# Performance work log

Measured on AMD Instinct MI355X. Metric: run time of the kernel, lower is better.

The kernel has to match this reference:

```python
import jax, jax.numpy as jnp
import numpy as np

D = 1024
H = 16
HD = D // H  # 64

def setup_inputs() -> dict:
    key = jax.random.key(0)
    ks = jax.random.split(key, 7)
    B, S = 2, 2048
    x = jax.random.normal(ks[0], (B, S, D), dtype=jnp.float32)
    M = jax.random.randint(ks[1], (B, S, S), 0, 2, dtype=jnp.int32)
    s = 1.0 / np.sqrt(D)
    W_q = jax.random.normal(ks[2], (D, D), dtype=jnp.float32) * s
    W_k = jax.random.normal(ks[3], (D, D), dtype=jnp.float32) * s
    W_v = jax.random.normal(ks[4], (D, D), dtype=jnp.float32) * s
    W_o = jax.random.normal(ks[5], (D, D), dtype=jnp.float32) * s
    b_o = jax.random.normal(ks[6], (D,), dtype=jnp.float32) * 0.01
    return {"x": x, "M": M, "W_q": W_q, "W_k": W_k, "W_v": W_v, "W_o": W_o, "b_o": b_o}

def reference(x, M, W_q, W_k, W_v, W_o, b_o):
    B, S, _ = x.shape
    scale = HD ** -0.5
    # project and split heads: [B, H, S, HD]
    def heads(W):
        return (x @ W.T).reshape(B, S, H, HD).transpose(0, 2, 1, 3)
    Q, K, V = heads(W_q), heads(W_k), heads(W_v)
    scores = jnp.einsum('bhqd,bhkd->bhqk', Q, K) * scale
    mask = (M[:, None, :, :] == 0)  # broadcast over heads
    scores = jnp.where(mask, jnp.float32(-1e9), scores)
    A = jax.nn.softmax(scores, axis=-1)
    out = jnp.einsum('bhqk,bhkd->bhqd', A, V)
    out = out.transpose(0, 2, 1, 3).reshape(B, S, D)
    return out @ W_o.T + b_o
```

## Files before the change

### kernel.cpp

```cpp
#include <hip/hip_runtime.h>
#include <hip/hip_bf16.h>

typedef unsigned short u16;
typedef unsigned int u32;
typedef unsigned long long u64;
typedef _Float16 f16;
typedef __attribute__((__ext_vector_type__(4))) _Float16 f16x4;
typedef __attribute__((__ext_vector_type__(8))) short bf16x8;
typedef __attribute__((__ext_vector_type__(4))) float f32x4;
typedef __attribute__((__ext_vector_type__(16))) float f32x16;

__device__ __forceinline__ u16 f2bf(float f) {
    u32 u = __float_as_uint(f);
    return (u16)((u + 0x7fffu + ((u >> 16) & 1u)) >> 16);
}

__device__ __forceinline__ u32 pk2(float e, float o) {
    return (__float_as_uint(e) >> 16) | (__float_as_uint(o) & 0xFFFF0000u);
}

__global__ __launch_bounds__(256) void prep_kernel(
    const float4* __restrict__ x,  const float4* __restrict__ wq,
    const float4* __restrict__ wk, const float4* __restrict__ wv,
    const float4* __restrict__ wo,
    u16* __restrict__ xb, u16* __restrict__ wqb, u16* __restrict__ wkb,
    u16* __restrict__ wvb, u16* __restrict__ wob,
    const int* __restrict__ M, u64* __restrict__ Mb2)
{
    if (blockIdx.x < 8192) {
        int gid = blockIdx.x * 256 + threadIdx.x;
        const float4* src; u16* dst; int off;
        if (gid < 1048576) { src = x; dst = xb; off = gid; }
        else {
            int g = gid - 1048576;
            int sel = g >> 18;
            off = g & 262143;
            src = sel == 0 ? wq : sel == 1 ? wk : sel == 2 ? wv : wo;
            dst = sel == 0 ? wqb : sel == 1 ? wkb : sel == 2 ? wvb : wob;
        }
        float4 f = src[off];
        ushort4 o;
        o.x = f2bf(f.x); o.y = f2bf(f.y); o.z = f2bf(f.z); o.w = f2bf(f.w);
        ((ushort4*)dst)[off] = o;
    } else {
        int wg   = (blockIdx.x - 8192) * 4 + (threadIdx.x >> 6);
        int lane = threadIdx.x & 63;
        int w = wg & 31;
        int q = (wg >> 5) & 2047;
        int b = wg >> 16;
        size_t base = ((size_t)(b * 2048 + q)) * 2048 + w * 64 + lane;
        u64 bits = __ballot(M[base] != 0);
        if (lane == 0) Mb2[(size_t)(b * 32 + w) * 2048 + q] = bits;
    }
}

template<int MODE, int BN>
__global__ __launch_bounds__(256) void gemm_k(
    const u16* __restrict__ Ag, const u16* __restrict__ Bg,
    u16* __restrict__ Cq, u16* __restrict__ Kfr, u16* __restrict__ Vfr,
    float* __restrict__ Cf, const float* __restrict__ bias)
{
    constexpr int Kd = 1024;
    constexpr int NB = BN / 32;
    __shared__ u16 As[128 * 32];
    __shared__ u16 Bs[BN * 32];
    const int tid  = threadIdx.x;
    const int wave = tid >> 6, lane = tid & 63;
    const int quad = lane >> 4, l16 = lane & 15;
    const int n0 = blockIdx.x * BN;
    const int m0 = blockIdx.y * 128;

    const int wm = (wave & 1) * 64, wn = (wave >> 1) * (BN / 2);
    f32x4 acc[4][NB];
    #pragma unroll
    for (int i = 0; i < 4; i++)
        #pragma unroll
        for (int j = 0; j < NB; j++)
            acc[i][j] = (f32x4){0.f, 0.f, 0.f, 0.f};

    const int sr = lane >> 2;
    const int sk = (lane & 3) * 8;
    const int ca0 = wave * 2, ca1 = ca0 + 1;
    const u16* gA0 = Ag + (size_t)(m0 + ca0 * 16 + sr) * Kd + sk;
    const u16* gA1 = Ag + (size_t)(m0 + ca1 * 16 + sr) * Kd + sk;
    u16* lA0 = As + ca0 * 512;
    u16* lA1 = As + ca1 * 512;
    const int cb0 = (BN == 128) ? wave * 2 : wave;
    const u16* gB0 = Bg + (size_t)(n0 + cb0 * 16 + sr) * Kd + sk;
    u16* lB0 = Bs + cb0 * 512;
    const u16* gB1 = (BN == 128) ? Bg + (size_t)(n0 + (cb0 + 1) * 16 + sr) * Kd + sk : nullptr;
    u16* lB1 = (BN == 128) ? Bs + (cb0 + 1) * 512 : nullptr;

    #define GLL16(gp, lp) __builtin_amdgcn_global_load_lds( \
        (const __attribute__((address_space(1))) void*)(gp), \
        (__attribute__((address_space(3))) void*)(lp), 16, 0, 0)

    for (int k0 = 0; k0 < Kd; k0 += 32) {
        __syncthreads();
        GLL16(gA0 + k0, lA0);
        GLL16(gA1 + k0, lA1);
        GLL16(gB0 + k0, lB0);
        if (BN == 128) GLL16(gB1 + k0, lB1);
        __syncthreads();

        bf16x8 af[4], bfr[NB];
        #pragma unroll
        for (int mb = 0; mb < 4; mb++)
            af[mb] = *(const bf16x8*)&As[(wm + mb * 16 + l16) * 32 + quad * 8];
        #pragma unroll
        for (int nb = 0; nb < NB; nb++)
            bfr[nb] = *(const bf16x8*)&Bs[(wn + nb * 16 + l16) * 32 + quad * 8];
        #pragma unroll
        for (int mb = 0; mb < 4; mb++)
            #pragma unroll
            for (int nb = 0; nb < NB; nb++)
                acc[mb][nb] = __builtin_amdgcn_mfma_f32_16x16x32_bf16(
                    af[mb], bfr[nb], acc[mb][nb], 0, 0, 0);
    }
    #undef GLL16

    #pragma unroll
    for (int mb = 0; mb < 4; mb++) {
        #pragma unroll
        for (int nb = 0; nb < NB; nb++) {
            const int row  = m0 + wm + mb * 16 + quad * 4;
            const int col  = n0 + wn + nb * 16 + l16;
            if (MODE == 1) {
                #pragma unroll
                for (int r = 0; r < 4; r++)
                    Cf[(size_t)(row + r) * 1024 + col] = acc[mb][nb][r] + bias[col];
            } else {
                const int region = col >> 10;
                const int ccol = col & 1023;
                const int bb = row >> 11, srow = row & 2047;
                const int kt = srow >> 6;
                const int hh = ccol >> 6, dd = ccol & 63;
                if (region == 0) {
                    #pragma unroll
                    for (int r = 0; r < 4; r++)
                        Cq[(size_t)(row + r) * 1024 + ccol] =
                            f2bf(acc[mb][nb][r] * 0.18033688011112042f);
                } else if (region == 1) {
                    const int t = dd >> 4, hik = (dd >> 3) & 1, j = dd & 7;
                    #pragma unroll
                    for (int r = 0; r < 4; r++) {
                        const int km = (srow + r) & 63;
                        const int kn = km >> 5, l31k = km & 31;
                        const int lanek = hik * 32 + l31k;
                        Kfr[((((size_t)(bb * 16 + hh) * 32 + kt) * 8 + kn * 4 + t) * 64
                             + lanek) * 8 + j] = f2bf(acc[mb][nb][r]);
                    }
                } else {
                    const int kinb = srow & 63;
                    const int t = kinb >> 4, hiv = (kinb >> 3) & 1, jb = kinb & 7;
                    const int nd = dd >> 5, l31v = dd & 31;
                    const int lanev = hiv * 32 + l31v;
                    ushort4 pk;
                    pk.x = f2bf(acc[mb][nb][0]); pk.y = f2bf(acc[mb][nb][1]);
                    pk.z = f2bf(acc[mb][nb][2]); pk.w = f2bf(acc[mb][nb][3]);
                    *(ushort4*)&Vfr[((((size_t)(bb * 16 + hh) * 32 + kt) * 8 + nd * 4 + t) * 64
                                     + lanev) * 8 + jb] = pk;
                }
            }
        }
    }
}

__global__ __launch_bounds__(256) void attn_kernel(
    const u16* __restrict__ Qg, const u16* __restrict__ Kfr, const u16* __restrict__ Vfr,
    const u64* __restrict__ Mb2, f16* __restrict__ Opart, float* __restrict__ Lpart)
{
    const int qt = blockIdx.x >> 1;
    const int kh = blockIdx.x & 1;
    const int h  = blockIdx.y;
    const int b  = blockIdx.z;
    const int tid = threadIdx.x, wave = tid >> 6, lane = tid & 63;
    const int l31 = lane & 31, hi = lane >> 5;

    const int    qrow0 = qt * 128 + wave * 32;
    const int    bh    = b * 16 + h;

    bf16x8 qf[4];
    {
        const u16* qp = Qg + ((size_t)b * 2048 + qrow0 + l31) * 1024 + h * 64 + hi * 8;
        #pragma unroll
        for (int t = 0; t < 4; t++) qf[t] = *(const bf16x8*)(qp + t * 16);
    }

    const u16* kfp = Kfr + (size_t)bh * 131072 + lane * 8;
    const u16* vfp = Vfr + (size_t)bh * 131072 + lane * 8;

    f32x16 oacc0, oacc1;
    #pragma unroll
    for (int i = 0; i < 16; i++) { oacc0[i] = 0.f; oacc1[i] = 0.f; }
    float lsum = 0.f;

    const int kt0 = kh * 16;
    #pragma unroll 1
    for (int kt = kt0; kt < kt0 + 16; kt++) {
        const u64 mwv = Mb2[(size_t)(b * 32 + kt) * 2048 + qrow0 + l31];
        const u32 mlo = ((u32)mwv) >> (hi * 4);
        const u32 mhi = ((u32)(mwv >> 32)) >> (hi * 4);
        const size_t fb = (size_t)(kt * 8) * 512;

        #pragma unroll
        for (int ph = 0; ph < 2; ph++) {
            bf16x8 kf[4], vf[4];
            #pragma unroll
            for (int t = 0; t < 4; t++)
                kf[t] = *(const bf16x8*)(kfp + fb + (size_t)(ph * 4 + t) * 512);
            vf[0] = *(const bf16x8*)(vfp + fb + (size_t)(2 * ph) * 512);
            vf[1] = *(const bf16x8*)(vfp + fb + (size_t)(2 * ph + 1) * 512);
            vf[2] = *(const bf16x8*)(vfp + fb + (size_t)(4 + 2 * ph) * 512);
            vf[3] = *(const bf16x8*)(vfp + fb + (size_t)(4 + 2 * ph + 1) * 512);

            f32x16 s;
            #pragma unroll
            for (int i = 0; i < 16; i++) s[i] = 0.f;
            #pragma unroll
            for (int t = 0; t < 4; t++)
                s = __builtin_amdgcn_mfma_f32_32x32x16_bf16(kf[t], qf[t], s, 0, 0, 0);

            const u32 mm = ph ? mhi : mlo;
            #pragma unroll
            for (int reg = 0; reg < 16; reg++) {
                const int kb2 = (reg & 3) + 8 * (reg >> 2);
                float a = __builtin_amdgcn_exp2f(s[reg]);
                a = ((mm >> kb2) & 1u) ? a : 0.0f;
                s[reg] = a; lsum += a;
            }

            bf16x8 pb[2];
            #pragma unroll
            for (int fl = 0; fl < 2; fl++) {
                const int rb = 8 * fl;
                u32 a0 = pk2(s[rb], s[rb + 1]),     a1 = pk2(s[rb + 2], s[rb + 3]);
                u32 a2 = pk2(s[rb + 4], s[rb + 5]), a3 = pk2(s[rb + 6], s[rb + 7]);
                const u32 r0 = __shfl_xor(a0, 32);
                const u32 r1 = __shfl_xor(a1, 32);
                const u32 r2 = __shfl_xor(a2, 32);
                const u32 r3 = __shfl_xor(a3, 32);
                union { u32 u[4]; bf16x8 v; } fu;
                fu.u[0] = hi ? r2 : a0;
                fu.u[1] = hi ? r3 : a1;
                fu.u[2] = hi ? a2 : r0;
                fu.u[3] = hi ? a3 : r1;
                pb[fl] = fu.v;
            }

            oacc0 = __builtin_amdgcn_mfma_f32_32x32x16_bf16(vf[0], pb[0], oacc0, 0, 0, 0);
            oacc0 = __builtin_amdgcn_mfma_f32_32x32x16_bf16(vf[1], pb[1], oacc0, 0, 0, 0);
            oacc1 = __builtin_amdgcn_mfma_f32_32x32x16_bf16(vf[2], pb[0], oacc1, 0, 0, 0);
            oacc1 = __builtin_amdgcn_mfma_f32_32x32x16_bf16(vf[3], pb[1], oacc1, 0, 0, 0);
        }
    }

    lsum += __shfl_xor(lsum, 32);

    const size_t obase = ((size_t)(kh * 32 + bh) * 2048 + qrow0 + l31) * 64;
    #pragma unroll
    for (int tile = 0; tile < 2; tile++) {
        #pragma unroll
        for (int g = 0; g < 4; g++) {
            const int d0 = tile * 32 + g * 8 + hi * 4;
            f16x4 pkv;
            #pragma unroll
            for (int r = 0; r < 4; r++) {
                const int reg = g * 4 + r;
                pkv[r] = (f16)(tile == 0 ? oacc0[reg] : oacc1[reg]);
            }
            *(f16x4*)&Opart[obase + d0] = pkv;
        }
    }
    Lpart[(size_t)kh * 65536 + bh * 2048 + qrow0 + l31] = lsum;
}

__global__ __launch_bounds__(256) void merge_kernel(
    const f16* __restrict__ Opart, const float* __restrict__ Lpart,
    u16* __restrict__ AO)
{
    const int gid = blockIdx.x * 256 + threadIdx.x;
    const int c4 = gid & 15;
    const int q  = (gid >> 4) & 2047;
    const int bh = gid >> 15;
    const int b  = bh >> 4, h = bh & 15;

    const size_t pbase = ((size_t)bh * 2048 + q) * 64 + c4 * 4;
    f16x4 o0 = *(const f16x4*)&Opart[pbase];
    f16x4 o1 = *(const f16x4*)&Opart[(size_t)32 * 2048 * 64 + pbase];
    const float l = Lpart[(size_t)bh * 2048 + q] +
                    Lpart[(size_t)65536 + bh * 2048 + q];
    const float inv = 1.0f / l;

    ushort4 o;
    o.x = f2bf(((float)o0[0] + (float)o1[0]) * inv);
    o.y = f2bf(((float)o0[1] + (float)o1[1]) * inv);
    o.z = f2bf(((float)o0[2] + (float)o1[2]) * inv);
    o.w = f2bf(((float)o0[3] + (float)o1[3]) * inv);
    *(ushort4*)&AO[((size_t)b * 2048 + q) * 1024 + h * 64 + c4 * 4] = o;
}

extern "C" void kernel_launch(void* const* d_in, const int* in_sizes, int n_in,
                              void* d_out, int out_size, void* d_ws, size_t ws_size,
                              hipStream_t stream)
{
    const float* x  = (const float*)d_in[0];
    const int*   Mm = (const int*)d_in[1];
    const float* Wq = (const float*)d_in[2];
    const float* Wk = (const float*)d_in[3];
    const float* Wv = (const float*)d_in[4];
    const float* Wo = (const float*)d_in[5];
    const float* bo = (const float*)d_in[6];
    float* out = (float*)d_out;

    u16* ws  = (u16*)d_ws;
    u16* xb  = ws;
    u16* wqb = xb  + 4194304;
    u16* wkb = wqb + 1048576;
    u16* wvb = wkb + 1048576;
    u16* wob = wvb + 1048576;
    u16* Qb  = wob + 1048576;
    u16* Kfr = Qb  + 4194304;
    u16* Vfr = Kfr + 4194304;
    u16* AOb = Vfr + 4194304;
    u64* Mb2 = (u64*)(AOb + 4194304);
    f16* Opart = (f16*)(Mb2 + 131072);
    float* Lpart = (float*)(Opart + 8388608);

    prep_kernel<<<40960, 256, 0, stream>>>(
        (const float4*)x, (const float4*)Wq, (const float4*)Wk,
        (const float4*)Wv, (const float4*)Wo, xb, wqb, wkb, wvb, wob,
        Mm, Mb2);

    dim3 g1(24, 32, 1);
    gemm_k<0, 128><<<g1, 256, 0, stream>>>(xb, wqb, Qb, Kfr, Vfr, nullptr, nullptr);

    dim3 g2(32, 16, 2);
    attn_kernel<<<g2, 256, 0, stream>>>(Qb, Kfr, Vfr, Mb2, Opart, Lpart);

    merge_kernel<<<4096, 256, 0, stream>>>(Opart, Lpart, AOb);

    dim3 g3(16, 32, 1);
    gemm_k<1, 64><<<g3, 256, 0, stream>>>(AOb, wob, nullptr, nullptr, nullptr,
                                          out, bo);
}
```

Before: 246.2 us.

## Stage K/V fragment epilogue through LDS and shrink attention blocks to one wave

The QKV GEMM epilogue for the K and V regions now writes bf16 fragments into a shared-memory staging buffer in two passes and then copies them out with contiguous 16-byte stores, replacing scattered 2-byte global writes. Separately, the attention kernel goes from 4 waves per block over 128 query rows to a single wave over 32 rows, with four times as many blocks. This aims at better global write coalescing and finer-grained scheduling of attention work, at the cost of extra barriers in the GEMM epilogue and no sharing of K/V loads across waves.

```diff
diff --git a/kernel.cpp b/kernel.cpp
--- a/kernel.cpp
+++ b/kernel.cpp
@@ -62,8 +62,9 @@
 {
     constexpr int Kd = 1024;
     constexpr int NB = BN / 32;
-    __shared__ u16 As[128 * 32];
-    __shared__ u16 Bs[BN * 32];
+    __shared__ u16 SM[8192];
+    u16* As = SM;
+    u16* Bs = SM + 4096;
     const int tid  = threadIdx.x;
     const int wave = tid >> 6, lane = tid & 63;
     const int quad = lane >> 4, l16 = lane & 15;
@@ -119,54 +120,85 @@
     }
     #undef GLL16
 
-    #pragma unroll
-    for (int mb = 0; mb < 4; mb++) {
-        #pragma unroll
-        for (int nb = 0; nb < NB; nb++) {
-            const int row  = m0 + wm + mb * 16 + quad * 4;
-            const int col  = n0 + wn + nb * 16 + l16;
-            if (MODE == 1) {
+    if (MODE == 1) {
+        #pragma unroll
+        for (int mb = 0; mb < 4; mb++)
+            #pragma unroll
+            for (int nb = 0; nb < NB; nb++) {
+                const int row = m0 + wm + mb * 16 + quad * 4;
+                const int col = n0 + wn + nb * 16 + l16;
                 #pragma unroll
                 for (int r = 0; r < 4; r++)
                     Cf[(size_t)(row + r) * 1024 + col] = acc[mb][nb][r] + bias[col];
-            } else {
-                const int region = col >> 10;
-                const int ccol = col & 1023;
-                const int bb = row >> 11, srow = row & 2047;
-                const int kt = srow >> 6;
-                const int hh = ccol >> 6, dd = ccol & 63;
-                if (region == 0) {
-                    #pragma unroll
-                    for (int r = 0; r < 4; r++)
-                        Cq[(size_t)(row + r) * 1024 + ccol] =
-                            f2bf(acc[mb][nb][r] * 0.18033688011112042f);
-                } else if (region == 1) {
+            }
+        return;
+    }
+
+    const int region = n0 >> 10;
+    if (region == 0) {
+        #pragma unroll
+        for (int mb = 0; mb < 4; mb++)
+            #pragma unroll
+            for (int nb = 0; nb < NB; nb++) {
+                const int row = m0 + wm + mb * 16 + quad * 4;
+                const int ccol = (n0 & 1023) + wn + nb * 16 + l16;
+                #pragma unroll
+                for (int r = 0; r < 4; r++)
+                    Cq[(size_t)(row + r) * 1024 + ccol] =
+                        f2bf(acc[mb][nb][r] * 0.18033688011112042f);
+            }
+        return;
+    }
+
+    const int bb = m0 >> 11;
+    const int kt_base = (m0 & 2047) >> 6;
+    const int head_base = (n0 & 1023) >> 6;
+    u16* dst = (region == 1) ? Kfr : Vfr;
+    #pragma unroll
+    for (int pass = 0; pass < 2; pass++) {
+        __syncthreads();
+        #pragma unroll
+        for (int mb = 0; mb < 4; mb++) {
+            const int rowb = wm + mb * 16 + quad * 4;
+            if ((rowb >> 6) != pass) continue;
+            #pragma unroll
+            for (int nb = 0; nb < NB; nb++) {
+                const int ccol = wn + nb * 16 + l16;
+                const int h2 = ccol >> 6, dd = ccol & 63;
+                if (region == 1) {
                     const int t = dd >> 4, hik = (dd >> 3) & 1, j = dd & 7;
                     #pragma unroll
                     for (int r = 0; r < 4; r++) {
-                        const int km = (srow + r) & 63;
-                        const int kn = km >> 5, l31k = km & 31;
-                        const int lanek = hik * 32 + l31k;
-                        Kfr[((((size_t)(bb * 16 + hh) * 32 + kt) * 8 + kn * 4 + t) * 64
-                             + lanek) * 8 + j] = f2bf(acc[mb][nb][r]);
+                        const int km = (rowb + r) & 63;
+                        const int f = (km >> 5) * 4 + t;
+                        const int lanek = hik * 32 + (km & 31);
+                        SM[((h2 * 8 + f) * 64 + lanek) * 8 + j] = f2bf(acc[mb][nb][r]);
                     }
                 } else {
-                    const int kinb = srow & 63;
+                    const int kinb = rowb & 63;
                     const int t = kinb >> 4, hiv = (kinb >> 3) & 1, jb = kinb & 7;
-                    const int nd = dd >> 5, l31v = dd & 31;
-                    const int lanev = hiv * 32 + l31v;
+                    const int f = (dd >> 5) * 4 + t;
+                    const int lanev = hiv * 32 + (dd & 31);
                     ushort4 pk;
                     pk.x = f2bf(acc[mb][nb][0]); pk.y = f2bf(acc[mb][nb][1]);
                     pk.z = f2bf(acc[mb][nb][2]); pk.w = f2bf(acc[mb][nb][3]);
-                    *(ushort4*)&Vfr[((((size_t)(bb * 16 + hh) * 32 + kt) * 8 + nd * 4 + t) * 64
-                                     + lanev) * 8 + jb] = pk;
+                    *(ushort4*)&SM[((h2 * 8 + f) * 64 + lanev) * 8 + jb] = pk;
                 }
             }
         }
-    }
-}
-
-__global__ __launch_bounds__(256) void attn_kernel(
+        __syncthreads();
+        const int h2g = tid >> 7;
+        const int inner = (tid & 127) * 32;
+        const size_t gbase =
+            ((size_t)(bb * 16 + head_base + h2g) * 32 + kt_base + pass) * 4096;
+        #pragma unroll
+        for (int c = 0; c < 4; c++)
+            *(bf16x8*)&dst[gbase + inner + c * 8] =
+                *(const bf16x8*)&SM[h2g * 4096 + inner + c * 8];
+    }
+}
+
+__global__ __launch_bounds__(64) void attn_kernel(
     const u16* __restrict__ Qg, const u16* __restrict__ Kfr, const u16* __restrict__ Vfr,
     const u64* __restrict__ Mb2, f16* __restrict__ Opart, float* __restrict__ Lpart)
 {
@@ -174,11 +206,11 @@
     const int kh = blockIdx.x & 1;
     const int h  = blockIdx.y;
     const int b  = blockIdx.z;
-    const int tid = threadIdx.x, wave = tid >> 6, lane = tid & 63;
+    const int lane = threadIdx.x;
     const int l31 = lane & 31, hi = lane >> 5;
 
-    const int    qrow0 = qt * 128 + wave * 32;
-    const int    bh    = b * 16 + h;
+    const int qrow0 = qt * 32;
+    const int bh    = b * 16 + h;
 
     bf16x8 qf[4];
     {
@@ -335,8 +367,8 @@
     dim3 g1(24, 32, 1);
     gemm_k<0, 128><<<g1, 256, 0, stream>>>(xb, wqb, Qb, Kfr, Vfr, nullptr, nullptr);
 
-    dim3 g2(32, 16, 2);
-    attn_kernel<<<g2, 256, 0, stream>>>(Qb, Kfr, Vfr, Mb2, Opart, Lpart);
+    dim3 g2(128, 16, 2);
+    attn_kernel<<<g2, 64, 0, stream>>>(Qb, Kfr, Vfr, Mb2, Opart, Lpart);
 
     merge_kernel<<<4096, 256, 0, stream>>>(Opart, Lpart, AOb);
 
```

New measurement: 270.7 us. 1.1x slower.
